# Kernel optimization log

Measured on AMD Instinct MI355X. Metric: run time of the kernel, lower is better.

Reference implementation:

```python
import jax, jax.numpy as jnp
import numpy as np

B, T, D, H = 4, 2048, 1024, 16
Dh = D // H  # 64


def setup_inputs() -> dict:
    key = jax.random.key(0)
    ks = jax.random.split(key, 12)
    s = 1.0 / np.sqrt(D)
    return {
        "q": jax.random.normal(ks[0], (B, T, D), jnp.float32),
        "k": jax.random.normal(ks[1], (B, T, D), jnp.float32),
        "v": jax.random.normal(ks[2], (B, T, D), jnp.float32),
        "Wq": jax.random.normal(ks[3], (D, D), jnp.float32) * s,
        "bq": jnp.zeros((D,), jnp.float32),
        "Wk": jax.random.normal(ks[4], (D, D), jnp.float32) * s,
        "bk": jnp.zeros((D,), jnp.float32),
        "Wv": jax.random.normal(ks[5], (Dh, D), jnp.float32) * s,
        "bv": jnp.zeros((Dh,), jnp.float32),
        "Wo": jax.random.normal(ks[6], (D, D), jnp.float32) * s,
        "bo": jnp.zeros((D,), jnp.float32),
    }


def reference(q, k, v, Wq, bq, Wk, bk, Wv, bv, Wo, bo):
    # Projections (torch Linear: y = x @ W.T + b)
    Q = (q @ Wq.T + bq).reshape(B, T, H, Dh)   # [B,T,H,Dh]
    K = (k @ Wk.T + bk).reshape(B, T, H, Dh)   # [B,T,H,Dh]
    Vs = v @ Wv.T + bv                         # [B,T,Dh] shared across heads
    scale = 1.0 / np.sqrt(Dh).astype(np.float32)
    scores = jnp.einsum('bqhd,bkhd->bhqk', Q, K) * scale  # [B,H,T,T]
    attn = jax.nn.softmax(scores, axis=-1)
    # shared-V: broadcast V over heads
    out = jnp.einsum('bhqk,bkd->bqhd', attn, Vs)  # [B,T,H,Dh]
    out = out.reshape(B, T, D)
    y = out @ Wo.T + bo                           # [B,T,D]
    return y, attn.mean(axis=1)                   # per-head-averaged attention
```

## Files before the change

### kernel.cpp

```cpp
#include <hip/hip_runtime.h>
#include <cstdint>
#include <cstddef>

typedef __attribute__((ext_vector_type(8))) _Float16 half8;
typedef __attribute__((ext_vector_type(4))) _Float16 half4;
typedef __attribute__((ext_vector_type(4))) float f32x4;

#define DEV static __device__ __forceinline__
#define AS1(p) (const __attribute__((address_space(1))) void*)(p)
#define AS3(p) (__attribute__((address_space(3))) void*)(p)

DEV half8 cvt8(const float* p) {
    f32x4 a = *(const f32x4*)p;
    f32x4 b = *(const f32x4*)(p + 4);
    half8 o;
    o[0] = (_Float16)a[0]; o[1] = (_Float16)a[1];
    o[2] = (_Float16)a[2]; o[3] = (_Float16)a[3];
    o[4] = (_Float16)b[0]; o[5] = (_Float16)b[1];
    o[6] = (_Float16)b[2]; o[7] = (_Float16)b[3];
    return o;
}

__global__ __launch_bounds__(256)
void cvt2_kernel(const float* __restrict__ a, _Float16* __restrict__ oa,
                 const float* __restrict__ b, _Float16* __restrict__ ob, int n8)
{
    int i = blockIdx.x * 256 + threadIdx.x;
    int stride = gridDim.x * 256;
    for (; i < 2 * n8; i += stride) {
        if (i < n8) ((half8*)oa)[i] = cvt8(a + (size_t)i * 8);
        else        ((half8*)ob)[i - n8] = cvt8(b + (size_t)(i - n8) * 8);
    }
}

__global__ __launch_bounds__(256)
void cvt3_kernel(const float* __restrict__ a, _Float16* __restrict__ oa,
                 const float* __restrict__ b, _Float16* __restrict__ ob,
                 const float* __restrict__ c, _Float16* __restrict__ oc, int n8)
{
    int i = blockIdx.x * 256 + threadIdx.x;
    int stride = gridDim.x * 256;
    for (; i < 3 * n8; i += stride) {
        if (i < n8)           ((half8*)oa)[i] = cvt8(a + (size_t)i * 8);
        else if (i < 2 * n8)  ((half8*)ob)[i - n8] = cvt8(b + (size_t)(i - n8) * 8);
        else                  ((half8*)oc)[i - 2 * n8] = cvt8(c + (size_t)(i - 2 * n8) * 8);
    }
}

__global__ __launch_bounds__(256)
void combine_kernel(const _Float16* __restrict__ a, const _Float16* __restrict__ b,
                    float* __restrict__ out, int n8)
{
    int i = blockIdx.x * 256 + threadIdx.x;
    int stride = gridDim.x * 256;
    for (; i < n8; i += stride) {
        half8 x = ((const half8*)a)[i];
        half8 y = ((const half8*)b)[i];
        f32x4 o0, o1;
#pragma unroll
        for (int j = 0; j < 4; j++) o0[j] = ((float)x[j] + (float)y[j]) * 0.0625f;
#pragma unroll
        for (int j = 0; j < 4; j++) o1[j] = ((float)x[j + 4] + (float)y[j + 4]) * 0.0625f;
        *(f32x4*)(out + (size_t)i * 8) = o0;
        *(f32x4*)(out + (size_t)i * 8 + 4) = o1;
    }
}

template<bool OUT_F16>
__global__ __launch_bounds__(256, 2)
void gemm16(const _Float16* __restrict__ A, const _Float16* __restrict__ B,
            const float* __restrict__ bias, float scale, void* __restrict__ Cout,
            int M, int N, int K)
{
    __shared__ half8 As[2][512];
    __shared__ half8 Bs[2][512];
    const int tid = threadIdx.x, l = tid & 63, w = tid >> 6;
    const int lr = l & 15, lh = l >> 4;
    const int wm0 = (w >> 1) * 64, wn0 = (w & 1) * 64;
    const int bm0 = blockIdx.x * 128, bn0 = blockIdx.y * 128;
    const int nsteps = K >> 5;

    f32x4 acc[4][4] = {};

#define STAGE(buf, t) do {                                                        \
        int k0 = (t) << 5;                                                        \
        _Pragma("unroll")                                                         \
        for (int q2 = 0; q2 < 2; q2++) {                                          \
            int r = q2 * 64 + l;                                                  \
            __builtin_amdgcn_global_load_lds(                                     \
                AS1(A + (size_t)(bm0 + r) * K + k0 + w * 8),                      \
                AS3(&As[buf][w * 128 + q2 * 64]), 16, 0, 0);                      \
            __builtin_amdgcn_global_load_lds(                                     \
                AS1(B + (size_t)(bn0 + r) * K + k0 + w * 8),                      \
                AS3(&Bs[buf][w * 128 + q2 * 64]), 16, 0, 0);                      \
        }                                                                         \
    } while (0)

    STAGE(0, 0);
    __syncthreads();
    for (int t = 0; t < nsteps; t++) {
        int cur = t & 1;
        if (t + 1 < nsteps) STAGE(cur ^ 1, t + 1);
        half8 a[4], b[4];
#pragma unroll
        for (int m = 0; m < 4; m++) a[m] = As[cur][lh * 128 + wm0 + m * 16 + lr];
#pragma unroll
        for (int n = 0; n < 4; n++) b[n] = Bs[cur][lh * 128 + wn0 + n * 16 + lr];
#pragma unroll
        for (int m = 0; m < 4; m++)
#pragma unroll
            for (int n = 0; n < 4; n++)
                acc[m][n] = __builtin_amdgcn_mfma_f32_16x16x32_f16(a[m], b[n], acc[m][n], 0, 0, 0);
        __syncthreads();
    }
#undef STAGE

#pragma unroll
    for (int m = 0; m < 4; m++)
#pragma unroll
        for (int n = 0; n < 4; n++) {
            int row0 = bm0 + wm0 + m * 16 + lh * 4;
            int col = bn0 + wn0 + n * 16 + lr;
            float bv = bias[col];
#pragma unroll
            for (int j = 0; j < 4; j++) {
                float val = (acc[m][n][j] + bv) * scale;
                int row = row0 + j;
                if constexpr (OUT_F16)
                    ((_Float16*)Cout)[(size_t)row * N + col] = (_Float16)val;
                else
                    ((float*)Cout)[(size_t)row * N + col] = val;
            }
        }
}

template<int BM, int BN, int WR, int WC>
__global__ __launch_bounds__(256, 2)
void gemm_vp(const float* __restrict__ Aptr, const float* __restrict__ Bw,
             const float* __restrict__ bias, _Float16* __restrict__ Cout, int M, int N, int K)
{
    constexpr int BK = 32;
    constexpr int WM = BM / WR, WN = BN / WC;
    constexpr int MF = WM / 16, NF = WN / 16;
    constexpr int LDT = 40;
    __shared__ _Float16 Asl[BM][LDT];
    __shared__ _Float16 Bsl[BN][LDT];

    const int tid = threadIdx.x;
    const int l = tid & 63;
    const int w = tid >> 6;
    const int wr = w / WC, wc = w % WC;
    const int lr = l & 15, lh = l >> 4;
    const int bm0 = blockIdx.y * BM, bn0 = blockIdx.x * BN;

    f32x4 acc[MF][NF] = {};

    for (int k0 = 0; k0 < K; k0 += BK) {
        __syncthreads();
        for (int c = tid; c < BM * 4; c += 256) {
            int row = c >> 2, c8 = (c & 3) << 3;
            *(half8*)&Asl[row][c8] = cvt8(Aptr + (size_t)(bm0 + row) * K + k0 + c8);
        }
        for (int c = tid; c < BN * 4; c += 256) {
            int row = c >> 2, c8 = (c & 3) << 3;
            *(half8*)&Bsl[row][c8] = cvt8(Bw + (size_t)(bn0 + row) * K + k0 + c8);
        }
        __syncthreads();

        half8 a[MF], b[NF];
#pragma unroll
        for (int m = 0; m < MF; m++)
            a[m] = *(const half8*)&Asl[wr * WM + m * 16 + lr][lh * 8];
#pragma unroll
        for (int n = 0; n < NF; n++)
            b[n] = *(const half8*)&Bsl[wc * WN + n * 16 + lr][lh * 8];
#pragma unroll
        for (int m = 0; m < MF; m++)
#pragma unroll
            for (int n = 0; n < NF; n++)
                acc[m][n] = __builtin_amdgcn_mfma_f32_16x16x32_f16(a[m], b[n], acc[m][n], 0, 0, 0);
    }

#pragma unroll
    for (int m = 0; m < MF; m++)
#pragma unroll
        for (int n = 0; n < NF; n++) {
            int row0 = bm0 + wr * WM + m * 16 + lh * 4;
            int col = bn0 + wc * WN + n * 16 + lr;
            float bv = bias[col];
#pragma unroll
            for (int j = 0; j < 4; j++) {
                float val = acc[m][n][j] + bv;
                int row = row0 + j;
                int bi = row >> 11, t = row & 2047;
                Cout[(((size_t)(bi * 64 + col)) << 11) + t] = (_Float16)val;
            }
        }
}

#define LK(dst, kt) do {                                                          \
        const _Float16* kp_ = Kb + (size_t)((kt) * 32) * 1024;                    \
        _Pragma("unroll")                                                         \
        for (int kfr_ = 0; kfr_ < 2; kfr_++)                                      \
            _Pragma("unroll")                                                     \
            for (int dk_ = 0; dk_ < 2; dk_++)                                     \
                dst[kfr_][dk_] = *(const half8*)(kp_ + (size_t)(kfr_ * 16 + lr) * 1024 \
                                                 + ch + dk_ * 32 + lh * 8);       \
    } while (0)

__global__ __launch_bounds__(512, 4)
void stats_kernel(const _Float16* __restrict__ Qh, const _Float16* __restrict__ Kh,
                  float* __restrict__ slp)
{
    const int blk = blockIdx.x;
    const int b = blk & 3;
    const int hg = (blk >> 2) & 1;
    const int q0 = (blk >> 3) << 5;
    const int tid = threadIdx.x;
    const int l = tid & 63, w = tid >> 6;
    const int lr = l & 15, lh = l >> 4;
    const int ch = (hg * 8 + w) * 64;

    const size_t base = (size_t)b * 2048 * 1024;
    const _Float16* Qb = Qh + base;
    const _Float16* Kb = Kh + base;

    half8 qf[2][2];
#pragma unroll
    for (int m = 0; m < 2; m++)
#pragma unroll
        for (int dk = 0; dk < 2; dk++)
            qf[m][dk] = *(const half8*)(Qb + (size_t)(q0 + m * 16 + lr) * 1024
                                        + ch + dk * 32 + lh * 8);

    float sl[2][4] = {};
    half8 ka[2][2], kb2[2][2];

#define SBODY(KF) do {                                                            \
        f32x4 sc[2][2] = {};                                                      \
        _Pragma("unroll")                                                         \
        for (int m = 0; m < 2; m++)                                               \
            _Pragma("unroll")                                                     \
            for (int kfr = 0; kfr < 2; kfr++)                                     \
                _Pragma("unroll")                                                 \
                for (int dk = 0; dk < 2; dk++)                                    \
                    sc[m][kfr] = __builtin_amdgcn_mfma_f32_16x16x32_f16(          \
                        qf[m][dk], KF[kfr][dk], sc[m][kfr], 0, 0, 0);             \
        _Pragma("unroll")                                                         \
        for (int m = 0; m < 2; m++)                                               \
            _Pragma("unroll")                                                     \
            for (int j = 0; j < 4; j++)                                           \
                sl[m][j] += __builtin_amdgcn_exp2f(sc[m][0][j])                   \
                          + __builtin_amdgcn_exp2f(sc[m][1][j]);                  \
    } while (0)

    LK(ka, 0);
    for (int kt = 0; kt < 64; kt += 2) {
        LK(kb2, kt + 1);
        SBODY(ka);
        LK(ka, kt + 2 < 64 ? kt + 2 : 63);
        SBODY(kb2);
    }
#undef SBODY

#pragma unroll
    for (int m = 0; m < 2; m++)
#pragma unroll
        for (int j = 0; j < 4; j++) {
            float s = sl[m][j];
#pragma unroll
            for (int d = 1; d < 16; d <<= 1)
                s += __shfl_xor(s, d, 64);
            if (lr == 0)
                slp[(size_t)(b * 16 + hg * 8 + w) * 2048 + q0 + m * 16 + lh * 4 + j] = s;
        }
}

__global__ __launch_bounds__(512, 4)
void emit_kernel(const _Float16* __restrict__ Qh, const _Float16* __restrict__ Kh,
                 const _Float16* __restrict__ VT, const float* __restrict__ slp,
                 _Float16* __restrict__ attnp, _Float16* __restrict__ Op)
{
    const int blk = blockIdx.x;
    const int b = blk & 3;
    const int hg = (blk >> 2) & 1;
    const int q0 = (blk >> 3) << 5;
    const int tid = threadIdx.x;
    const int l = tid & 63, w = tid >> 6;
    const int lr = l & 15, lh = l >> 4;
    const int ch = (hg * 8 + w) * 64;

    __shared__ __align__(16) _Float16 Pld[2][8][32][40];

    const size_t base = (size_t)b * 2048 * 1024;
    const _Float16* Qb = Qh + base;
    const _Float16* Kb = Kh + base;

    half8 qf[2][2];
#pragma unroll
    for (int m = 0; m < 2; m++)
#pragma unroll
        for (int dk = 0; dk < 2; dk++)
            qf[m][dk] = *(const half8*)(Qb + (size_t)(q0 + m * 16 + lr) * 1024
                                        + ch + dk * 32 + lh * 8);

    float rinv[2];
    {
        const float* sr = slp + (size_t)(b * 16 + hg * 8 + w) * 2048 + q0;
#pragma unroll
        for (int m = 0; m < 2; m++)
            rinv[m] = 1.0f / sr[m * 16 + lr];
    }

    f32x4 oacc[2][4] = {};
    half8 ka[2][2], kb2[2][2];

#define EBODY(KF, KT, P) do {                                                     \
        const int krow = (KT) * 32;                                               \
        f32x4 sc[2][2] = {};         \
        _Pragma("unroll")                                                         \
        for (int m = 0; m < 2; m++)                                               \
            _Pragma("unroll")                                                     \
            for (int kfr = 0; kfr < 2; kfr++)                                     \
                _Pragma("unroll")                                                 \
                for (int dk = 0; dk < 2; dk++)                                    \
                    sc[m][kfr] = __builtin_amdgcn_mfma_f32_16x16x32_f16(          \
                        KF[kfr][dk], qf[m][dk], sc[m][kfr], 0, 0, 0);             \
        _Pragma("unroll")                                                         \
        for (int m = 0; m < 2; m++)                                               \
            _Pragma("unroll")                                                     \
            for (int kfr = 0; kfr < 2; kfr++) {                                   \
                half4 pk4;                                                        \
                _Pragma("unroll")                                                 \
                for (int j = 0; j < 4; j++)                                       \
                    pk4[j] = (_Float16)(__builtin_amdgcn_exp2f(sc[m][kfr][j])     \
                                        * rinv[m]);                               \
                *(half4*)&Pld[P][w][m * 16 + lr][kfr * 16 + lh * 4] = pk4;        \
            }                                                                     \
        half8 vf[4], pa[2];                                                       \
        _Pragma("unroll")                                                         \
        for (int dv = 0; dv < 4; dv++)                                            \
            vf[dv] = *(const half8*)(VT + (((size_t)(b * 64 + dv * 16 + lr)) << 11) + krow + lh * 8); \
        _Pragma("unroll")                                                         \
        for (int m = 0; m < 2; m++)                                               \
            pa[m] = *(const half8*)&Pld[P][w][m * 16 + lr][lh * 8];               \
        _Pragma("unroll")                                                         \
        for (int m = 0; m < 2; m++)                                               \
            _Pragma("unroll")                                                     \
            for (int dv = 0; dv < 4; dv++)                                        \
                oacc[m][dv] = __builtin_amdgcn_mfma_f32_16x16x32_f16(             \
                    pa[m], vf[dv], oacc[m][dv], 0, 0, 0);                         \
        __syncthreads();                                                          \
        {                                                                         \
            int r = tid >> 4, c2 = (tid & 15) * 2;                                \
            float s0 = 0.f, s1 = 0.f;                                             \
            _Pragma("unroll")                                                     \
            for (int ww = 0; ww < 8; ww++) {                                      \
                union { uint32_t u; _Float16 h[2]; } pv;                          \
                pv.u = *(const uint32_t*)&Pld[P][ww][r][c2];                      \
                s0 += (float)pv.h[0]; s1 += (float)pv.h[1];                       \
            }                                                                     \
            union { _Float16 h[2]; uint32_t u; } pk;                              \
            pk.h[0] = (_Float16)s0; pk.h[1] = (_Float16)s1;                       \
            __builtin_nontemporal_store(pk.u, (uint32_t*)(attnp                   \
                + (size_t)hg * 16777216 + (((size_t)(b * 2048 + q0 + r)) << 11)   \
                + krow + c2));                                                    \
        }                                                                         \
    } while (0)

    LK(ka, 0);
    for (int i = 0; i < 64; i += 2) {
        LK(kb2, i + 1);
        EBODY(ka, i, 0);
        LK(ka, i + 2 < 64 ? i + 2 : 63);
        EBODY(kb2, i + 1, 1);
    }
#undef EBODY

    _Float16* op = Op + base;
#pragma unroll
    for (int m = 0; m < 2; m++)
#pragma unroll
        for (int dv = 0; dv < 4; dv++)
#pragma unroll
            for (int j = 0; j < 4; j++) {
                int row = q0 + m * 16 + lh * 4 + j;
                int col = ch + dv * 16 + lr;
                op[(size_t)row * 1024 + col] = (_Float16)oacc[m][dv][j];
            }
}

extern "C" void kernel_launch(void* const* d_in, const int* in_sizes, int n_in,
                              void* d_out, int out_size, void* d_ws, size_t ws_size,
                              hipStream_t stream)
{
    const float* q  = (const float*)d_in[0];
    const float* k  = (const float*)d_in[1];
    const float* v  = (const float*)d_in[2];
    const float* Wq = (const float*)d_in[3];
    const float* bq = (const float*)d_in[4];
    const float* Wk = (const float*)d_in[5];
    const float* bk = (const float*)d_in[6];
    const float* Wv = (const float*)d_in[7];
    const float* bv = (const float*)d_in[8];
    const float* Wo = (const float*)d_in[9];
    const float* bo = (const float*)d_in[10];

    float* y = (float*)d_out;
    float* attn_mean = y + (size_t)4 * 2048 * 1024;

    uint8_t* ws = (uint8_t*)d_ws;
    _Float16* Qh  = (_Float16*)(ws);
    _Float16* Kh  = (_Float16*)(ws + 16777216);
    _Float16* VT  = (_Float16*)(ws + 33554432);
    _Float16* Wqc = (_Float16*)(ws + 34603008);
    _Float16* Wkc = (_Float16*)(ws + 36700160);
    _Float16* Woc = (_Float16*)(ws + 38797312);
    _Float16* qc  = (_Float16*)(ws + 40894464);
    _Float16* kc  = (_Float16*)(ws + 57671680);
    _Float16* Op  = qc;
    _Float16* attnp = (_Float16*)(ws + 74448896);
    float*    slp = (float*)(ws + 34603008);

    const float QS = 0.125f * 1.44269504088896340736f;

    cvt2_kernel<<<dim3(2048), dim3(256), 0, stream>>>(q, qc, k, kc, 1048576);
    cvt3_kernel<<<dim3(512),  dim3(256), 0, stream>>>(Wq, Wqc, Wk, Wkc, Wo, Woc, 131072);

    gemm16<true><<<dim3(64, 8), dim3(256), 0, stream>>>(qc, Wqc, bq, QS, Qh, 8192, 1024, 1024);
    gemm16<true><<<dim3(64, 8), dim3(256), 0, stream>>>(kc, Wkc, bk, 1.0f, Kh, 8192, 1024, 1024);
    gemm_vp<128, 64, 4, 1><<<dim3(1, 64), dim3(256), 0, stream>>>(v, Wv, bv, VT, 8192, 64, 1024);

    stats_kernel<<<dim3(512), dim3(512), 0, stream>>>(Qh, Kh, slp);
    emit_kernel<<<dim3(512), dim3(512), 0, stream>>>(Qh, Kh, VT, slp, attnp, Op);

    combine_kernel<<<dim3(2048), dim3(256), 0, stream>>>(
        attnp, attnp + (size_t)16777216, attn_mean, 2097152);

    gemm16<false><<<dim3(64, 8), dim3(256), 0, stream>>>(Op, Woc, bo, 1.0f, y, 8192, 1024, 1024);
}
```

Measured before the change: 570.2 us.

## Halve emit-kernel barriers by processing two key tiles per sync and add MFMA priority

The emit loop is restructured so that each iteration computes QK and writes probabilities for two key tiles into a quadruple-buffered shared array, then does both PV updates, followed by a single barrier and a combined head-sum store of the attention rows. This halves the number of __syncthreads per key sweep and lets the V loads overlap the QK work. s_setprio is also raised around the MFMA blocks in both the sum and emit kernels to favour matrix issue. The cost is double the LDS footprint for the P buffer, which may reduce occupancy at 512 threads with 4 blocks requested.

```diff
diff --git a/kernel.cpp b/kernel.cpp
--- a/kernel.cpp
+++ b/kernel.cpp
@@ -238,6 +238,7 @@
 
 #define SBODY(KF) do {                                                            \
         f32x4 sc[2][2] = {};                                                      \
+        __builtin_amdgcn_s_setprio(1);                                            \
         _Pragma("unroll")                                                         \
         for (int m = 0; m < 2; m++)                                               \
             _Pragma("unroll")                                                     \
@@ -246,6 +247,7 @@
                 for (int dk = 0; dk < 2; dk++)                                    \
                     sc[m][kfr] = __builtin_amdgcn_mfma_f32_16x16x32_f16(          \
                         qf[m][dk], KF[kfr][dk], sc[m][kfr], 0, 0, 0);             \
+        __builtin_amdgcn_s_setprio(0);                                            \
         _Pragma("unroll")                                                         \
         for (int m = 0; m < 2; m++)                                               \
             _Pragma("unroll")                                                     \
@@ -290,7 +292,7 @@
     const int lr = l & 15, lh = l >> 4;
     const int ch = (hg * 8 + w) * 64;
 
-    __shared__ __align__(16) _Float16 Pld[2][8][32][40];
+    __shared__ __align__(16) _Float16 Pld[2][2][8][32][40];
 
     const size_t base = (size_t)b * 2048 * 1024;
     const _Float16* Qb = Qh + base;
@@ -315,9 +317,9 @@
     f32x4 oacc[2][4] = {};
     half8 ka[2][2], kb2[2][2];
 
-#define EBODY(KF, KT, P) do {                                                     \
-        const int krow = (KT) * 32;                                               \
-        f32x4 sc[2][2] = {};         \
+#define QKW(KF, PAR, SLOT) do {                                                   \
+        f32x4 sc[2][2] = {};                                                      \
+        __builtin_amdgcn_s_setprio(1);                                            \
         _Pragma("unroll")                                                         \
         for (int m = 0; m < 2; m++)                                               \
             _Pragma("unroll")                                                     \
@@ -326,6 +328,7 @@
                 for (int dk = 0; dk < 2; dk++)                                    \
                     sc[m][kfr] = __builtin_amdgcn_mfma_f32_16x16x32_f16(          \
                         KF[kfr][dk], qf[m][dk], sc[m][kfr], 0, 0, 0);             \
+        __builtin_amdgcn_s_setprio(0);                                            \
         _Pragma("unroll")                                                         \
         for (int m = 0; m < 2; m++)                                               \
             _Pragma("unroll")                                                     \
@@ -335,47 +338,69 @@
                 for (int j = 0; j < 4; j++)                                       \
                     pk4[j] = (_Float16)(__builtin_amdgcn_exp2f(sc[m][kfr][j])     \
                                         * rinv[m]);                               \
-                *(half4*)&Pld[P][w][m * 16 + lr][kfr * 16 + lh * 4] = pk4;        \
+                *(half4*)&Pld[PAR][SLOT][w][m * 16 + lr][kfr * 16 + lh * 4] = pk4;\
             }                                                                     \
-        half8 vf[4], pa[2];                                                       \
+    } while (0)
+
+#define LVF(KT) do {                                                              \
         _Pragma("unroll")                                                         \
         for (int dv = 0; dv < 4; dv++)                                            \
-            vf[dv] = *(const half8*)(VT + (((size_t)(b * 64 + dv * 16 + lr)) << 11) + krow + lh * 8); \
-        _Pragma("unroll")                                                         \
-        for (int m = 0; m < 2; m++)                                               \
-            pa[m] = *(const half8*)&Pld[P][w][m * 16 + lr][lh * 8];               \
+            vf[dv] = *(const half8*)(VT + (((size_t)(b * 64 + dv * 16 + lr)) << 11) \
+                                     + (KT) * 32 + lh * 8);                       \
+    } while (0)
+
+#define PVS(PAR, SLOT) do {                                                       \
+        half8 pa[2];                                                              \
+        _Pragma("unroll")                                                         \
+        for (int m = 0; m < 2; m++)                                               \
+            pa[m] = *(const half8*)&Pld[PAR][SLOT][w][m * 16 + lr][lh * 8];       \
+        __builtin_amdgcn_s_setprio(1);                                            \
         _Pragma("unroll")                                                         \
         for (int m = 0; m < 2; m++)                                               \
             _Pragma("unroll")                                                     \
             for (int dv = 0; dv < 4; dv++)                                        \
                 oacc[m][dv] = __builtin_amdgcn_mfma_f32_16x16x32_f16(             \
                     pa[m], vf[dv], oacc[m][dv], 0, 0, 0);                         \
-        __syncthreads();                                                          \
-        {                                                                         \
-            int r = tid >> 4, c2 = (tid & 15) * 2;                                \
-            float s0 = 0.f, s1 = 0.f;                                             \
-            _Pragma("unroll")                                                     \
-            for (int ww = 0; ww < 8; ww++) {                                      \
-                union { uint32_t u; _Float16 h[2]; } pv;                          \
-                pv.u = *(const uint32_t*)&Pld[P][ww][r][c2];                      \
-                s0 += (float)pv.h[0]; s1 += (float)pv.h[1];                       \
-            }                                                                     \
-            union { _Float16 h[2]; uint32_t u; } pk;                              \
-            pk.h[0] = (_Float16)s0; pk.h[1] = (_Float16)s1;                       \
-            __builtin_nontemporal_store(pk.u, (uint32_t*)(attnp                   \
-                + (size_t)hg * 16777216 + (((size_t)(b * 2048 + q0 + r)) << 11)   \
-                + krow + c2));                                                    \
-        }                                                                         \
+        __builtin_amdgcn_s_setprio(0);                                            \
     } while (0)
 
     LK(ka, 0);
-    for (int i = 0; i < 64; i += 2) {
-        LK(kb2, i + 1);
-        EBODY(ka, i, 0);
-        LK(ka, i + 2 < 64 ? i + 2 : 63);
-        EBODY(kb2, i + 1, 1);
-    }
-#undef EBODY
+    for (int si = 0; si < 32; si++) {
+        const int par = si & 1;
+        const int kt0 = 2 * si, kt1 = 2 * si + 1;
+        half8 vf[4];
+        LK(kb2, kt1);
+        LVF(kt0);
+        QKW(ka, par, 0);
+        LK(ka, kt1 + 1 < 64 ? kt1 + 1 : 63);
+        QKW(kb2, par, 1);
+        PVS(par, 0);
+        LVF(kt1);
+        PVS(par, 1);
+        __syncthreads();
+        {
+            const int r = tid >> 4, c2 = (tid & 15) * 2;
+            const size_t arow = (size_t)hg * 16777216
+                              + (((size_t)(b * 2048 + q0 + r)) << 11) + c2;
+#pragma unroll
+            for (int slot = 0; slot < 2; slot++) {
+                float s0 = 0.f, s1 = 0.f;
+#pragma unroll
+                for (int ww = 0; ww < 8; ww++) {
+                    union { uint32_t u; _Float16 h[2]; } pv;
+                    pv.u = *(const uint32_t*)&Pld[par][slot][ww][r][c2];
+                    s0 += (float)pv.h[0]; s1 += (float)pv.h[1];
+                }
+                union { _Float16 h[2]; uint32_t u; } pk;
+                pk.h[0] = (_Float16)s0; pk.h[1] = (_Float16)s1;
+                __builtin_nontemporal_store(pk.u,
+                    (uint32_t*)(attnp + arow + (2 * si + slot) * 32));
+            }
+        }
+    }
+#undef QKW
+#undef LVF
+#undef PVS
 
     _Float16* op = Op + base;
 #pragma unroll
```

Result: slower. 682.2 us (+19.6%).
